# Kernel optimization log

Measured on AMD Instinct MI355X. Metric: run time of the kernel, lower is better.

## Reference

```python
import jax, jax.numpy as jnp
import numpy as np

N_ATOMS = 50000
N_PAIRS = 800000
N_EMB = 128
N_DIST = 100
N_HID = 128


def _glorot(key, shape):
    scale = jnp.sqrt(2.0 / (shape[0] + shape[1])).astype(jnp.float32)
    return jax.random.normal(key, shape, dtype=jnp.float32) * scale


def setup_inputs() -> dict:
    key = jax.random.key(0)
    ks = jax.random.split(key, 10)
    atom_features = jax.random.normal(ks[0], (N_ATOMS, N_EMB), dtype=jnp.float32)
    distance = jax.random.uniform(ks[1], (N_PAIRS, N_DIST), dtype=jnp.float32)
    atom_membership = jax.random.randint(ks[2], (N_ATOMS,), 0, 64, dtype=jnp.int32)
    distance_membership_i = jnp.sort(
        jax.random.randint(ks[3], (N_PAIRS,), 0, N_ATOMS, dtype=jnp.int32))
    distance_membership_j = jax.random.randint(ks[4], (N_PAIRS,), 0, N_ATOMS, dtype=jnp.int32)
    W_cf = _glorot(ks[5], (N_EMB, N_HID))
    W_df = _glorot(ks[6], (N_DIST, N_HID))
    W_fc = _glorot(ks[7], (N_HID, N_EMB))
    # original inits biases to zero; use small random so the b_df*afh branch is non-trivial
    b_cf = jax.random.normal(ks[8], (N_HID,), dtype=jnp.float32) * 0.1
    b_df = jax.random.normal(ks[9], (N_HID,), dtype=jnp.float32) * 0.1
    return {
        "atom_features": atom_features,
        "distance": distance,
        "atom_membership": atom_membership,
        "distance_membership_i": distance_membership_i,
        "distance_membership_j": distance_membership_j,
        "W_cf": W_cf, "W_df": W_df, "W_fc": W_fc,
        "b_cf": b_cf, "b_df": b_df,
    }


def reference(atom_features, distance, atom_membership,
              distance_membership_i, distance_membership_j,
              W_cf, W_df, W_fc, b_cf, b_df):
    n_atoms = atom_features.shape[0]
    # [n_pairs, n_hidden]
    distance_hidden = distance @ W_df + b_df
    # [n_atoms, n_hidden]
    atom_features_hidden = atom_features @ W_cf + b_cf
    # gather source-atom hidden feats per pair, fuse with distance feats
    msgs = distance_hidden * atom_features_hidden[distance_membership_j]
    msgs = jnp.tanh(msgs @ W_fc)                      # [n_pairs, n_emb]
    # self-interaction correction term
    output_ii = jnp.tanh((b_df * atom_features_hidden) @ W_fc)  # [n_atoms, n_emb]
    agg = jax.ops.segment_sum(msgs, distance_membership_i, num_segments=n_atoms)
    return agg - output_ii + atom_features
```

## Files before the change

### kernel.cpp

```cpp
#include <hip/hip_runtime.h>
#include <hip/hip_bf16.h>

#define N_ATOMS 50000
#define N_PAIRS 800000
#define N_EMB   128
#define N_DIST  100
#define N_HID   128
#define TP      128

typedef __attribute__((ext_vector_type(8))) short bf16x8;
typedef __attribute__((ext_vector_type(4))) float f32x4;

__device__ __forceinline__ short f2b(float x) {
  union { float f; unsigned u; } v; v.f = x;
  unsigned r = (v.u + 0x7FFF + ((v.u >> 16) & 1)) >> 16;
  return (short)r;
}
__device__ __forceinline__ float b2f(short b) {
  union { unsigned u; float f; } v; v.u = ((unsigned)(unsigned short)b) << 16;
  return v.f;
}
__device__ __forceinline__ float fast_tanh(float x) {
  const float z = __builtin_amdgcn_exp2f(x * 2.8853900817779268f);
  return 1.f - 2.f * __builtin_amdgcn_rcpf(z + 1.f);
}

__device__ __forceinline__ int frag_idx(int k, int n) {
  return ((((k >> 5) * 8 + (n >> 4)) * 64) + (((k >> 3) & 3) * 16) + (n & 15)) * 8 + (k & 7);
}

__device__ __forceinline__ void g2lds16(const void* g, void* l) {
  __builtin_amdgcn_global_load_lds(
      (const __attribute__((address_space(1))) unsigned*)g,
      (__attribute__((address_space(3))) unsigned*)l, 16, 0, 0);
}
__device__ __forceinline__ void stage_weights(const short* __restrict__ src,
                                              short* WS, int tid) {
  #pragma unroll
  for (int r = 0; r < 4; ++r) {
    const int off = (r * 512 + tid) * 8;
    g2lds16(src + off, WS + off);
  }
}

__global__ __launch_bounds__(256) void prep_kernel(
    const float* __restrict__ Wcf, const float* __restrict__ Wdf,
    const float* __restrict__ Wfc, short* __restrict__ Wcf_f,
    short* __restrict__ Wdf_f, short* __restrict__ Wfc_f) {
  const int e = blockIdx.x * 256 + threadIdx.x;
  const int k = e >> 7, n = e & 127;
  const int fi = frag_idx(k, n);
  Wcf_f[fi] = f2b(Wcf[k * N_HID + n]);
  Wfc_f[fi] = f2b(Wfc[k * N_EMB + n]);
  Wdf_f[fi] = (k < N_DIST) ? f2b(Wdf[k * N_HID + n]) : (short)0;
}

__global__ __launch_bounds__(512) void afh_kernel(
    const float* __restrict__ af, const short* __restrict__ Wcf_f,
    const float* __restrict__ bcf, float* __restrict__ afh) {
  __shared__ short WS[128 * 128];
  const int tid = threadIdx.x;
  const int lane = tid & 63, w = tid >> 6;
  const int lane15 = lane & 15, quad = lane >> 4;
  const int a0 = blockIdx.x * 128;

  stage_weights(Wcf_f, WS, tid);

  f32x4 acc[8];
  #pragma unroll
  for (int nt = 0; nt < 8; ++nt) {
    const float b = bcf[nt * 16 + lane15];
    acc[nt] = (f32x4){b, b, b, b};
  }
  const int arow = min(a0 + w * 16 + lane15, N_ATOMS - 1);
  const float* __restrict__ p = af + (long)arow * N_EMB;
  __syncthreads();

  for (int ks = 0; ks < 4; ++ks) {
    const int k0 = ks * 32 + quad * 8;
    const float4 x = *(const float4*)(p + k0);
    const float4 y = *(const float4*)(p + k0 + 4);
    bf16x8 a;
    a[0] = f2b(x.x); a[1] = f2b(x.y); a[2] = f2b(x.z); a[3] = f2b(x.w);
    a[4] = f2b(y.x); a[5] = f2b(y.y); a[6] = f2b(y.z); a[7] = f2b(y.w);
    #pragma unroll
    for (int nt = 0; nt < 8; ++nt) {
      const bf16x8 b = *(const bf16x8*)&WS[((ks * 8 + nt) * 64 + lane) * 8];
      acc[nt] = __builtin_amdgcn_mfma_f32_16x16x32_bf16(a, b, acc[nt], 0, 0, 0);
    }
  }
  #pragma unroll
  for (int reg = 0; reg < 4; ++reg) {
    const int row = a0 + w * 16 + quad * 4 + reg;
    if (row < N_ATOMS) {
      #pragma unroll
      for (int nt = 0; nt < 8; ++nt)
        afh[(long)row * N_HID + nt * 16 + lane15] = acc[nt][reg];
    }
  }
}

__global__ __launch_bounds__(512, 4) void pair_kernel(
    const float* __restrict__ dist, const int* __restrict__ mi,
    const int* __restrict__ mj, const short* __restrict__ Wdf_f,
    const short* __restrict__ Wfc_f, const float* __restrict__ bdf,
    const float* __restrict__ afh, float* __restrict__ agg) {
  __shared__ short WS[128 * 128];
  __shared__ short HS[TP * 128];

  const int tid = threadIdx.x;
  const int lane = tid & 63;
  const int w = tid >> 6;
  const int lane15 = lane & 15;
  const int quad = lane >> 4;
  const long pbase = (long)blockIdx.x * TP;
  const int R = w * 16;

  stage_weights(Wdf_f, WS, tid);

  float g[4][8];
  #pragma unroll
  for (int reg = 0; reg < 4; ++reg) {
    const int r = R + quad * 4 + reg;
    const long j = mj[pbase + r];
    const float* __restrict__ arow = afh + j * N_HID + lane15;
    #pragma unroll
    for (int nt = 0; nt < 8; ++nt)
      g[reg][nt] = arow[nt * 16];
  }

  const float* __restrict__ drow = dist + (pbase + R + lane15) * (long)N_DIST;
  float4 dx[4], dy[4];
  #pragma unroll
  for (int ks = 0; ks < 3; ++ks) {
    const int k0 = ks * 32 + quad * 8;
    dx[ks] = *(const float4*)(drow + k0);
    dy[ks] = *(const float4*)(drow + k0 + 4);
  }
  {
    const float4 z = {0.f, 0.f, 0.f, 0.f};
    dx[3] = (quad == 0) ? *(const float4*)(drow + 96) : z;
    dy[3] = z;
  }

  f32x4 acc[8];
  #pragma unroll
  for (int nt = 0; nt < 8; ++nt) {
    const float b = bdf[nt * 16 + lane15];
    acc[nt] = (f32x4){b, b, b, b};
  }
  __syncthreads();

  #pragma unroll
  for (int ks = 0; ks < 4; ++ks) {
    bf16x8 a;
    a[0] = f2b(dx[ks].x); a[1] = f2b(dx[ks].y);
    a[2] = f2b(dx[ks].z); a[3] = f2b(dx[ks].w);
    a[4] = f2b(dy[ks].x); a[5] = f2b(dy[ks].y);
    a[6] = f2b(dy[ks].z); a[7] = f2b(dy[ks].w);
    #pragma unroll
    for (int nt = 0; nt < 8; ++nt) {
      const bf16x8 b = *(const bf16x8*)&WS[((ks * 8 + nt) * 64 + lane) * 8];
      acc[nt] = __builtin_amdgcn_mfma_f32_16x16x32_bf16(a, b, acc[nt], 0, 0, 0);
    }
  }
  __syncthreads();

  stage_weights(Wfc_f, WS, tid);

  #pragma unroll
  for (int reg = 0; reg < 4; ++reg) {
    const int r = R + quad * 4 + reg;
    #pragma unroll
    for (int nt = 0; nt < 8; ++nt) {
      const int col = nt * 16 + lane15;
      const float h = acc[nt][reg] * g[reg][nt];
      const int ch = (col >> 3) ^ (r & 15);
      HS[(r << 7) + (ch << 3) + (col & 7)] = f2b(h);
    }
  }
  __syncthreads();

  f32x4 acc2[8];
  #pragma unroll
  for (int nt = 0; nt < 8; ++nt) acc2[nt] = (f32x4){0.f, 0.f, 0.f, 0.f};
  const int m = R + lane15;
  #pragma unroll
  for (int ks = 0; ks < 4; ++ks) {
    const int ch = (ks * 4 + quad) ^ lane15;
    const bf16x8 a = *(const bf16x8*)&HS[(m << 7) + (ch << 3)];
    #pragma unroll
    for (int nt = 0; nt < 8; ++nt) {
      const bf16x8 b = *(const bf16x8*)&WS[((ks * 8 + nt) * 64 + lane) * 8];
      acc2[nt] = __builtin_amdgcn_mfma_f32_16x16x32_bf16(a, b, acc2[nt], 0, 0, 0);
    }
  }

  #pragma unroll
  for (int reg = 0; reg < 4; ++reg) {
    const int r = R + quad * 4 + reg;
    #pragma unroll
    for (int nt = 0; nt < 8; ++nt) {
      const int col = nt * 16 + lane15;
      const float tv = fast_tanh(acc2[nt][reg]);
      const int ch = (col >> 3) ^ (r & 15);
      HS[(r << 7) + (ch << 3) + (col & 7)] = f2b(tv);
    }
  }
  __builtin_amdgcn_wave_barrier();

  {
    const int c0 = lane * 2;
    const long p0 = pbase + R;
    float s0 = 0.f, s1 = 0.f;
    int cur = mi[p0];
    for (int rr = 0; rr < 16; ++rr) {
      const int r = R + rr;
      const int idx = mi[p0 + rr];
      if (idx != cur) {
        atomicAdd(&agg[(size_t)cur * N_EMB + c0], s0);
        atomicAdd(&agg[(size_t)cur * N_EMB + c0 + 1], s1);
        s0 = s1 = 0.f; cur = idx;
      }
      const int ch = (c0 >> 3) ^ (r & 15);
      const unsigned v =
          *(const unsigned*)&HS[(r << 7) + (ch << 3) + (c0 & 7)];
      s0 += b2f((short)(v & 0xFFFF));
      s1 += b2f((short)(v >> 16));
    }
    atomicAdd(&agg[(size_t)cur * N_EMB + c0], s0);
    atomicAdd(&agg[(size_t)cur * N_EMB + c0 + 1], s1);
  }
}

__global__ __launch_bounds__(512) void out_kernel(
    const float* __restrict__ af, const float* __restrict__ afh,
    const short* __restrict__ Wfc_f, const float* __restrict__ bdf,
    const float* __restrict__ agg, float* __restrict__ out) {
  __shared__ short WS[128 * 128];
  const int tid = threadIdx.x;
  const int lane = tid & 63, w = tid >> 6;
  const int lane15 = lane & 15, quad = lane >> 4;
  const int a0 = blockIdx.x * 128;

  stage_weights(Wfc_f, WS, tid);

  f32x4 acc[8];
  #pragma unroll
  for (int nt = 0; nt < 8; ++nt) acc[nt] = (f32x4){0.f, 0.f, 0.f, 0.f};
  const int arow = min(a0 + w * 16 + lane15, N_ATOMS - 1);
  const float* __restrict__ p = afh + (long)arow * N_HID;
  __syncthreads();

  for (int ks = 0; ks < 4; ++ks) {
    const int k0 = ks * 32 + quad * 8;
    const float4 x = *(const float4*)(p + k0);
    const float4 y = *(const float4*)(p + k0 + 4);
    const float4 bx = *(const float4*)(bdf + k0);
    const float4 by = *(const float4*)(bdf + k0 + 4);
    bf16x8 a;
    a[0] = f2b(x.x * bx.x); a[1] = f2b(x.y * bx.y);
    a[2] = f2b(x.z * bx.z); a[3] = f2b(x.w * bx.w);
    a[4] = f2b(y.x * by.x); a[5] = f2b(y.y * by.y);
    a[6] = f2b(y.z * by.z); a[7] = f2b(y.w * by.w);
    #pragma unroll
    for (int nt = 0; nt < 8; ++nt) {
      const bf16x8 b = *(const bf16x8*)&WS[((ks * 8 + nt) * 64 + lane) * 8];
      acc[nt] = __builtin_amdgcn_mfma_f32_16x16x32_bf16(a, b, acc[nt], 0, 0, 0);
    }
  }
  #pragma unroll
  for (int reg = 0; reg < 4; ++reg) {
    const int row = a0 + w * 16 + quad * 4 + reg;
    if (row < N_ATOMS) {
      #pragma unroll
      for (int nt = 0; nt < 8; ++nt) {
        const size_t idx = (size_t)row * N_EMB + nt * 16 + lane15;
        out[idx] = agg[idx] - fast_tanh(acc[nt][reg]) + af[idx];
      }
    }
  }
}

extern "C" void kernel_launch(void* const* d_in, const int* in_sizes, int n_in,
                              void* d_out, int out_size, void* d_ws, size_t ws_size,
                              hipStream_t stream) {
  const float* af   = (const float*)d_in[0];
  const float* dist = (const float*)d_in[1];
  const int*   mi   = (const int*)d_in[3];
  const int*   mj   = (const int*)d_in[4];
  const float* Wcf  = (const float*)d_in[5];
  const float* Wdf  = (const float*)d_in[6];
  const float* Wfc  = (const float*)d_in[7];
  const float* bcf  = (const float*)d_in[8];
  const float* bdf  = (const float*)d_in[9];
  float* out = (float*)d_out;

  float* afh = (float*)d_ws;
  float* agg = afh + (size_t)N_ATOMS * N_HID;
  short* Wcf_f = (short*)(agg + (size_t)N_ATOMS * N_EMB);
  short* Wdf_f = Wcf_f + 128 * 128;
  short* Wfc_f = Wdf_f + 128 * 128;

  hipMemsetAsync(agg, 0, (size_t)N_ATOMS * N_EMB * sizeof(float), stream);
  prep_kernel<<<64, 256, 0, stream>>>(Wcf, Wdf, Wfc, Wcf_f, Wdf_f, Wfc_f);
  afh_kernel<<<(N_ATOMS + 127) / 128, 512, 0, stream>>>(af, Wcf_f, bcf, afh);
  pair_kernel<<<N_PAIRS / TP, 512, 0, stream>>>(dist, mi, mj, Wdf_f, Wfc_f, bdf, afh, agg);
  out_kernel<<<(N_ATOMS + 127) / 128, 512, 0, stream>>>(af, afh, Wfc_f, bdf, agg, out);
}
```

Before: 601.5 us.

## Fuse self-interaction into afh kernel, accumulate pairs into output, drop LDS weights

The self-interaction term is now computed inside the atom-hidden kernel, which writes af minus tanh directly into the output. The pair kernel then atomically adds messages straight into the output, removing the agg buffer, its memset and the final out kernel. The pair kernel also reads the bf16 weight fragments from global/L2 instead of staging them into LDS, which drops block-wide barriers and raises the occupancy hint to 6. It remaps block IDs for XCD locality and raises wave priority around the MFMA loops. The cost is more global/L2 traffic for weight reads in every wave.

```diff
diff --git a/kernel.cpp b/kernel.cpp
--- a/kernel.cpp
+++ b/kernel.cpp
@@ -55,10 +55,13 @@
   Wdf_f[fi] = (k < N_DIST) ? f2b(Wdf[k * N_HID + n]) : (short)0;
 }
 
-__global__ __launch_bounds__(512) void afh_kernel(
+__global__ __launch_bounds__(512) void afh_out_kernel(
     const float* __restrict__ af, const short* __restrict__ Wcf_f,
-    const float* __restrict__ bcf, float* __restrict__ afh) {
+    const short* __restrict__ Wfc_f, const float* __restrict__ bcf,
+    const float* __restrict__ bdf, float* __restrict__ afh,
+    float* __restrict__ out) {
   __shared__ short WS[128 * 128];
+  __shared__ short HS[128 * 128];
   const int tid = threadIdx.x;
   const int lane = tid & 63, w = tid >> 6;
   const int lane15 = lane & 15, quad = lane >> 4;
@@ -89,23 +92,57 @@
       acc[nt] = __builtin_amdgcn_mfma_f32_16x16x32_bf16(a, b, acc[nt], 0, 0, 0);
     }
   }
+  __syncthreads();
+
+  stage_weights(Wfc_f, WS, tid);
+
+  #pragma unroll
+  for (int reg = 0; reg < 4; ++reg) {
+    const int lr = w * 16 + quad * 4 + reg;
+    const int row = a0 + lr;
+    #pragma unroll
+    for (int nt = 0; nt < 8; ++nt) {
+      const int col = nt * 16 + lane15;
+      const float v = acc[nt][reg];
+      if (row < N_ATOMS) afh[(long)row * N_HID + col] = v;
+      const int ch = (col >> 3) ^ (lr & 15);
+      HS[(lr << 7) + (ch << 3) + (col & 7)] = f2b(v * bdf[col]);
+    }
+  }
+  __syncthreads();
+
+  f32x4 acc2[8];
+  #pragma unroll
+  for (int nt = 0; nt < 8; ++nt) acc2[nt] = (f32x4){0.f, 0.f, 0.f, 0.f};
+  const int m = w * 16 + lane15;
+  #pragma unroll
+  for (int ks = 0; ks < 4; ++ks) {
+    const int ch = (ks * 4 + quad) ^ lane15;
+    const bf16x8 a = *(const bf16x8*)&HS[(m << 7) + (ch << 3)];
+    #pragma unroll
+    for (int nt = 0; nt < 8; ++nt) {
+      const bf16x8 b = *(const bf16x8*)&WS[((ks * 8 + nt) * 64 + lane) * 8];
+      acc2[nt] = __builtin_amdgcn_mfma_f32_16x16x32_bf16(a, b, acc2[nt], 0, 0, 0);
+    }
+  }
   #pragma unroll
   for (int reg = 0; reg < 4; ++reg) {
     const int row = a0 + w * 16 + quad * 4 + reg;
     if (row < N_ATOMS) {
       #pragma unroll
-      for (int nt = 0; nt < 8; ++nt)
-        afh[(long)row * N_HID + nt * 16 + lane15] = acc[nt][reg];
-    }
-  }
-}
-
-__global__ __launch_bounds__(512, 4) void pair_kernel(
+      for (int nt = 0; nt < 8; ++nt) {
+        const size_t idx = (size_t)row * N_EMB + nt * 16 + lane15;
+        out[idx] = af[idx] - fast_tanh(acc2[nt][reg]);
+      }
+    }
+  }
+}
+
+__global__ __launch_bounds__(512, 6) void pair_kernel(
     const float* __restrict__ dist, const int* __restrict__ mi,
     const int* __restrict__ mj, const short* __restrict__ Wdf_f,
     const short* __restrict__ Wfc_f, const float* __restrict__ bdf,
-    const float* __restrict__ afh, float* __restrict__ agg) {
-  __shared__ short WS[128 * 128];
+    const float* __restrict__ afh, float* __restrict__ out) {
   __shared__ short HS[TP * 128];
 
   const int tid = threadIdx.x;
@@ -113,88 +150,90 @@
   const int w = tid >> 6;
   const int lane15 = lane & 15;
   const int quad = lane >> 4;
-  const long pbase = (long)blockIdx.x * TP;
   const int R = w * 16;
 
-  stage_weights(Wdf_f, WS, tid);
-
-  float g[4][8];
+  const int nwg = gridDim.x;
+  const int q = nwg >> 3, rr8 = nwg & 7;
+  const int xcd = blockIdx.x & 7, slot = blockIdx.x >> 3;
+  const int wg = (xcd < rr8 ? xcd * (q + 1) : rr8 * (q + 1) + (xcd - rr8) * q) + slot;
+  const long pbase = (long)wg * TP;
+
+  const float* __restrict__ drow = dist + (pbase + R + lane15) * (long)N_DIST;
+  bf16x8 afr[4];
+  {
+    float4 x[4], y[3];
+    #pragma unroll
+    for (int ks = 0; ks < 3; ++ks) {
+      const int k0 = ks * 32 + quad * 8;
+      x[ks] = *(const float4*)(drow + k0);
+      y[ks] = *(const float4*)(drow + k0 + 4);
+    }
+    const float4 z = {0.f, 0.f, 0.f, 0.f};
+    x[3] = (quad == 0) ? *(const float4*)(drow + 96) : z;
+    #pragma unroll
+    for (int ks = 0; ks < 3; ++ks) {
+      afr[ks][0] = f2b(x[ks].x); afr[ks][1] = f2b(x[ks].y);
+      afr[ks][2] = f2b(x[ks].z); afr[ks][3] = f2b(x[ks].w);
+      afr[ks][4] = f2b(y[ks].x); afr[ks][5] = f2b(y[ks].y);
+      afr[ks][6] = f2b(y[ks].z); afr[ks][7] = f2b(y[ks].w);
+    }
+    afr[3][0] = f2b(x[3].x); afr[3][1] = f2b(x[3].y);
+    afr[3][2] = f2b(x[3].z); afr[3][3] = f2b(x[3].w);
+    afr[3][4] = 0; afr[3][5] = 0; afr[3][6] = 0; afr[3][7] = 0;
+  }
+
+  f32x4 acc[8];
+  #pragma unroll
+  for (int nt = 0; nt < 8; ++nt) {
+    const float b = bdf[nt * 16 + lane15];
+    acc[nt] = (f32x4){b, b, b, b};
+  }
+
+  __builtin_amdgcn_s_setprio(1);
+  #pragma unroll
+  for (int ks = 0; ks < 4; ++ks) {
+    #pragma unroll
+    for (int nt = 0; nt < 8; ++nt) {
+      const bf16x8 b = *(const bf16x8*)&Wdf_f[((ks * 8 + nt) * 64 + lane) * 8];
+      acc[nt] = __builtin_amdgcn_mfma_f32_16x16x32_bf16(afr[ks], b, acc[nt], 0, 0, 0);
+    }
+  }
+  __builtin_amdgcn_s_setprio(0);
+
   #pragma unroll
   for (int reg = 0; reg < 4; ++reg) {
     const int r = R + quad * 4 + reg;
     const long j = mj[pbase + r];
     const float* __restrict__ arow = afh + j * N_HID + lane15;
-    #pragma unroll
-    for (int nt = 0; nt < 8; ++nt)
-      g[reg][nt] = arow[nt * 16];
-  }
-
-  const float* __restrict__ drow = dist + (pbase + R + lane15) * (long)N_DIST;
-  float4 dx[4], dy[4];
-  #pragma unroll
-  for (int ks = 0; ks < 3; ++ks) {
-    const int k0 = ks * 32 + quad * 8;
-    dx[ks] = *(const float4*)(drow + k0);
-    dy[ks] = *(const float4*)(drow + k0 + 4);
-  }
-  {
-    const float4 z = {0.f, 0.f, 0.f, 0.f};
-    dx[3] = (quad == 0) ? *(const float4*)(drow + 96) : z;
-    dy[3] = z;
-  }
-
-  f32x4 acc[8];
-  #pragma unroll
-  for (int nt = 0; nt < 8; ++nt) {
-    const float b = bdf[nt * 16 + lane15];
-    acc[nt] = (f32x4){b, b, b, b};
-  }
-  __syncthreads();
-
-  #pragma unroll
-  for (int ks = 0; ks < 4; ++ks) {
-    bf16x8 a;
-    a[0] = f2b(dx[ks].x); a[1] = f2b(dx[ks].y);
-    a[2] = f2b(dx[ks].z); a[3] = f2b(dx[ks].w);
-    a[4] = f2b(dy[ks].x); a[5] = f2b(dy[ks].y);
-    a[6] = f2b(dy[ks].z); a[7] = f2b(dy[ks].w);
-    #pragma unroll
-    for (int nt = 0; nt < 8; ++nt) {
-      const bf16x8 b = *(const bf16x8*)&WS[((ks * 8 + nt) * 64 + lane) * 8];
-      acc[nt] = __builtin_amdgcn_mfma_f32_16x16x32_bf16(a, b, acc[nt], 0, 0, 0);
-    }
-  }
-  __syncthreads();
-
-  stage_weights(Wfc_f, WS, tid);
-
-  #pragma unroll
-  for (int reg = 0; reg < 4; ++reg) {
-    const int r = R + quad * 4 + reg;
+    float g[8];
+    #pragma unroll
+    for (int nt = 0; nt < 8; ++nt) g[nt] = arow[nt * 16];
     #pragma unroll
     for (int nt = 0; nt < 8; ++nt) {
       const int col = nt * 16 + lane15;
-      const float h = acc[nt][reg] * g[reg][nt];
+      const float h = acc[nt][reg] * g[nt];
       const int ch = (col >> 3) ^ (r & 15);
       HS[(r << 7) + (ch << 3) + (col & 7)] = f2b(h);
     }
   }
-  __syncthreads();
+  __builtin_amdgcn_wave_barrier();
 
   f32x4 acc2[8];
   #pragma unroll
   for (int nt = 0; nt < 8; ++nt) acc2[nt] = (f32x4){0.f, 0.f, 0.f, 0.f};
   const int m = R + lane15;
+  __builtin_amdgcn_s_setprio(1);
   #pragma unroll
   for (int ks = 0; ks < 4; ++ks) {
     const int ch = (ks * 4 + quad) ^ lane15;
     const bf16x8 a = *(const bf16x8*)&HS[(m << 7) + (ch << 3)];
     #pragma unroll
     for (int nt = 0; nt < 8; ++nt) {
-      const bf16x8 b = *(const bf16x8*)&WS[((ks * 8 + nt) * 64 + lane) * 8];
+      const bf16x8 b = *(const bf16x8*)&Wfc_f[((ks * 8 + nt) * 64 + lane) * 8];
       acc2[nt] = __builtin_amdgcn_mfma_f32_16x16x32_bf16(a, b, acc2[nt], 0, 0, 0);
     }
   }
+  __builtin_amdgcn_s_setprio(0);
 
   #pragma unroll
   for (int reg = 0; reg < 4; ++reg) {
@@ -218,8 +257,8 @@
       const int r = R + rr;
       const int idx = mi[p0 + rr];
       if (idx != cur) {
-        atomicAdd(&agg[(size_t)cur * N_EMB + c0], s0);
-        atomicAdd(&agg[(size_t)cur * N_EMB + c0 + 1], s1);
+        atomicAdd(&out[(size_t)cur * N_EMB + c0], s0);
+        atomicAdd(&out[(size_t)cur * N_EMB + c0 + 1], s1);
         s0 = s1 = 0.f; cur = idx;
       }
       const int ch = (c0 >> 3) ^ (r & 15);
@@ -228,57 +267,8 @@
       s0 += b2f((short)(v & 0xFFFF));
       s1 += b2f((short)(v >> 16));
     }
-    atomicAdd(&agg[(size_t)cur * N_EMB + c0], s0);
-    atomicAdd(&agg[(size_t)cur * N_EMB + c0 + 1], s1);
-  }
-}
-
-__global__ __launch_bounds__(512) void out_kernel(
-    const float* __restrict__ af, const float* __restrict__ afh,
-    const short* __restrict__ Wfc_f, const float* __restrict__ bdf,
-    const float* __restrict__ agg, float* __restrict__ out) {
-  __shared__ short WS[128 * 128];
-  const int tid = threadIdx.x;
-  const int lane = tid & 63, w = tid >> 6;
-  const int lane15 = lane & 15, quad = lane >> 4;
-  const int a0 = blockIdx.x * 128;
-
-  stage_weights(Wfc_f, WS, tid);
-
-  f32x4 acc[8];
-  #pragma unroll
-  for (int nt = 0; nt < 8; ++nt) acc[nt] = (f32x4){0.f, 0.f, 0.f, 0.f};
-  const int arow = min(a0 + w * 16 + lane15, N_ATOMS - 1);
-  const float* __restrict__ p = afh + (long)arow * N_HID;
-  __syncthreads();
-
-  for (int ks = 0; ks < 4; ++ks) {
-    const int k0 = ks * 32 + quad * 8;
-    const float4 x = *(const float4*)(p + k0);
-    const float4 y = *(const float4*)(p + k0 + 4);
-    const float4 bx = *(const float4*)(bdf + k0);
-    const float4 by = *(const float4*)(bdf + k0 + 4);
-    bf16x8 a;
-    a[0] = f2b(x.x * bx.x); a[1] = f2b(x.y * bx.y);
-    a[2] = f2b(x.z * bx.z); a[3] = f2b(x.w * bx.w);
-    a[4] = f2b(y.x * by.x); a[5] = f2b(y.y * by.y);
-    a[6] = f2b(y.z * by.z); a[7] = f2b(y.w * by.w);
-    #pragma unroll
-    for (int nt = 0; nt < 8; ++nt) {
-      const bf16x8 b = *(const bf16x8*)&WS[((ks * 8 + nt) * 64 + lane) * 8];
-      acc[nt] = __builtin_amdgcn_mfma_f32_16x16x32_bf16(a, b, acc[nt], 0, 0, 0);
-    }
-  }
-  #pragma unroll
-  for (int reg = 0; reg < 4; ++reg) {
-    const int row = a0 + w * 16 + quad * 4 + reg;
-    if (row < N_ATOMS) {
-      #pragma unroll
-      for (int nt = 0; nt < 8; ++nt) {
-        const size_t idx = (size_t)row * N_EMB + nt * 16 + lane15;
-        out[idx] = agg[idx] - fast_tanh(acc[nt][reg]) + af[idx];
-      }
-    }
+    atomicAdd(&out[(size_t)cur * N_EMB + c0], s0);
+    atomicAdd(&out[(size_t)cur * N_EMB + c0 + 1], s1);
   }
 }
 
@@ -297,14 +287,13 @@
   float* out = (float*)d_out;
 
   float* afh = (float*)d_ws;
-  float* agg = afh + (size_t)N_ATOMS * N_HID;
-  short* Wcf_f = (short*)(agg + (size_t)N_ATOMS * N_EMB);
+  short* Wcf_f = (short*)(afh + (size_t)N_ATOMS * N_HID);
   short* Wdf_f = Wcf_f + 128 * 128;
   short* Wfc_f = Wdf_f + 128 * 128;
 
-  hipMemsetAsync(agg, 0, (size_t)N_ATOMS * N_EMB * sizeof(float), stream);
   prep_kernel<<<64, 256, 0, stream>>>(Wcf, Wdf, Wfc, Wcf_f, Wdf_f, Wfc_f);
-  afh_kernel<<<(N_ATOMS + 127) / 128, 512, 0, stream>>>(af, Wcf_f, bcf, afh);
-  pair_kernel<<<N_PAIRS / TP, 512, 0, stream>>>(dist, mi, mj, Wdf_f, Wfc_f, bdf, afh, agg);
-  out_kernel<<<(N_ATOMS + 127) / 128, 512, 0, stream>>>(af, afh, Wfc_f, bdf, agg, out);
-}
+  afh_out_kernel<<<(N_ATOMS + 127) / 128, 512, 0, stream>>>(
+      af, Wcf_f, Wfc_f, bcf, bdf, afh, out);
+  pair_kernel<<<N_PAIRS / TP, 512, 0, stream>>>(
+      dist, mi, mj, Wdf_f, Wfc_f, bdf, afh, out);
+}
```

After: 800.5 us. 1.33x slower.
